# Performance work log

Hardware: AMD Instinct MI355X
Metric: run time of the kernel (lower is better)

The kernel has to match this reference:

```python
import jax, jax.numpy as jnp
import numpy as np

SEQ = 400      # hardcoded per-batch node count in head_splitter
HEADS = 10     # hardcoded num_heads
EPS = 1e-5     # torch LayerNorm default eps


def setup_inputs() -> dict:
    key = jax.random.key(0)
    ks = jax.random.split(key, 6)
    in_dim = out_dim = 640
    N = 25600  # 64 batches * 400 nodes
    x = jax.random.normal(ks[0], (N, in_dim), dtype=jnp.float32)
    # nn.Linear(in, out, bias=False) weights have shape [out, in]; y = x @ W.T
    s = 1.0 / np.sqrt(in_dim)
    Wq = jax.random.uniform(ks[1], (out_dim, in_dim), jnp.float32, -s, s)
    Wk = jax.random.uniform(ks[2], (out_dim, in_dim), jnp.float32, -s, s)
    Wv = jax.random.uniform(ks[3], (out_dim, in_dim), jnp.float32, -s, s)
    gamma = jnp.ones((out_dim,), jnp.float32)
    beta = jnp.zeros((out_dim,), jnp.float32)
    return {"x": x, "Wq": Wq, "Wk": Wk, "Wv": Wv, "gamma": gamma, "beta": beta}


def reference(x, Wq, Wk, Wv, gamma, beta):
    N, D = x.shape
    B = N // SEQ
    dk = D // HEADS
    Q = x @ Wq.T
    K = x @ Wk.T
    V = x @ Wv.T
    # head_splitter: per-batch raw reshape [SEQ, D] -> (HEADS, SEQ, dk), stacked
    # == raw reshape of the full contiguous tensor [N, D] -> (B, HEADS, SEQ, dk)
    Qh = Q.reshape(B, HEADS, SEQ, dk)
    Vh = V.reshape(B, HEADS, SEQ, dk)
    # NOTE: original uses torch.reshape (NOT transpose) to get (B, H, dk, SEQ)
    Kh = K.reshape(B, HEADS, SEQ, dk).reshape(B, HEADS, dk, SEQ)
    scale = 1.0 / jnp.sqrt(jnp.float32(dk))
    scores = jnp.einsum('bhqd,bhdk->bhqk', Qh, Kh) * scale  # [B,H,SEQ,SEQ]
    w = jax.nn.softmax(scores, axis=-1)
    vals = jnp.einsum('bhqk,bhkd->bhqd', w, Vh)  # [B,H,SEQ,dk]
    # raw row-major reshape back to [N, D], as in the original
    y = vals.reshape(N, D) + x
    mu = jnp.mean(y, axis=-1, keepdims=True)
    var = jnp.mean(jnp.square(y - mu), axis=-1, keepdims=True)
    return (y - mu) * jax.lax.rsqrt(var + EPS) * gamma + beta
```

## Files before the change

### kernel.cpp

```cpp
#include <hip/hip_runtime.h>
#include <hip/hip_bf16.h>


typedef unsigned short u16;
typedef short s8v __attribute__((ext_vector_type(8)));
typedef float f4v __attribute__((ext_vector_type(4)));
typedef u16  u4v __attribute__((ext_vector_type(4)));
typedef u16  u8v __attribute__((ext_vector_type(8)));

__device__ __forceinline__ float us2f(u16 u) {
    union { float f; unsigned int i; } v; v.i = ((unsigned int)u) << 16; return v.f;
}
__device__ __forceinline__ u16 f2us(float f) {
    __hip_bfloat16 h = __float2bfloat16(f);
    return *reinterpret_cast<u16*>(&h);
}
__device__ __forceinline__ s8v ld8f(const float* p) {
    const float4 a = ((const float4*)p)[0], b = ((const float4*)p)[1];
    s8v r;
    r[0] = (short)f2us(a.x); r[1] = (short)f2us(a.y);
    r[2] = (short)f2us(a.z); r[3] = (short)f2us(a.w);
    r[4] = (short)f2us(b.x); r[5] = (short)f2us(b.y);
    r[6] = (short)f2us(b.z); r[7] = (short)f2us(b.w);
    return r;
}
__device__ __forceinline__ void gload16(const u16* g, u16* l) {
    u16* gm = const_cast<u16*>(g);
    __builtin_amdgcn_global_load_lds(
        (__attribute__((address_space(1))) unsigned int*)gm,
        (__attribute__((address_space(3))) unsigned int*)l, 16, 0, 0);
}


__global__ __launch_bounds__(256)
void cvt(const float* __restrict__ Wq, const float* __restrict__ Wk,
         const float* __restrict__ Wv, const float* __restrict__ x,
         u16* __restrict__ Wb, u16* __restrict__ xb)
{
    const int g = blockIdx.x * 256 + threadIdx.x;
    if (g < 153600) {
        const float* src = (g < 51200) ? Wq : (g < 102400) ? Wk : Wv;
        const int rem = g % 51200;
        *(s8v*)(Wb + (size_t)g * 8) = ld8f(src + (size_t)rem * 8);
    } else {
        const int gx = g - 153600;
        *(s8v*)(xb + (size_t)gx * 8) = ld8f(x + (size_t)gx * 8);
    }
}

#define QKV_LDS 36864
__global__ __launch_bounds__(256, 4)
void qkv(const u16* __restrict__ xb, const u16* __restrict__ Wb,
         u16* __restrict__ Qb, u16* __restrict__ Kb, u16* __restrict__ Vb)
{
    extern __shared__ u16 qsm[];
    u16* As = qsm;
    u16* Bs = qsm + 8192;
    const int bx = blockIdx.x;
    const int sw = (bx & 7) * 375 + (bx >> 3);
    const int mt = sw / 15, nt = sw % 15;
    const int m0 = mt * 128, n0 = nt * 128;
    const int t = threadIdx.x, lane = t & 63, w = t >> 6;
    const int l15 = lane & 15, quad = lane >> 4;
    const int wr = w >> 1, wc = w & 1;

    f4v acc[4][4];
    #pragma unroll
    for (int a = 0; a < 4; ++a)
        #pragma unroll
        for (int b = 0; b < 4; ++b) acc[a][b] = (f4v){0.f, 0.f, 0.f, 0.f};

    for (int k0 = 0; k0 < 640; k0 += 64) {
        __syncthreads();
        #pragma unroll
        for (int j = 0; j < 4; ++j) {
            const int c  = (w * 4 + j) * 64 + lane;
            const int rg = c >> 3;
            const int sg = (c & 7) ^ (rg & 7);
            gload16(xb + (size_t)(m0 + rg) * 640 + k0 + sg * 8,
                    As + (w * 4 + j) * 512);
            gload16(Wb + (size_t)(n0 + rg) * 640 + k0 + sg * 8,
                    Bs + (w * 4 + j) * 512);
        }
        __syncthreads();

        #pragma unroll
        for (int kk = 0; kk < 2; ++kk) {
            s8v af[4], bf[4];
            #pragma unroll
            for (int mi = 0; mi < 4; ++mi) {
                const int row = wr * 64 + mi * 16 + l15;
                const int s   = kk * 4 + quad;
                af[mi] = *(const s8v*)(As + ((row * 8 + (s ^ (row & 7))) << 3));
            }
            #pragma unroll
            for (int ni = 0; ni < 4; ++ni) {
                const int row = wc * 64 + ni * 16 + l15;
                const int s   = kk * 4 + quad;
                bf[ni] = *(const s8v*)(Bs + ((row * 8 + (s ^ (row & 7))) << 3));
            }
            #pragma unroll
            for (int mi = 0; mi < 4; ++mi)
                #pragma unroll
                for (int ni = 0; ni < 4; ++ni)
                    acc[mi][ni] = __builtin_amdgcn_mfma_f32_16x16x32_bf16(
                        af[mi], bf[ni], acc[mi][ni], 0, 0, 0);
        }
    }

    __syncthreads();
    u16* Cs = qsm;
    #pragma unroll
    for (int mi = 0; mi < 4; ++mi)
        #pragma unroll
        for (int ni = 0; ni < 4; ++ni)
            #pragma unroll
            for (int i = 0; i < 4; ++i) {
                const int row = wr * 64 + mi * 16 + quad * 4 + i;
                const int col = wc * 64 + ni * 16 + l15;
                Cs[row * 144 + col] = f2us(acc[mi][ni][i]);
            }
    __syncthreads();
    const int mat = (n0 >= 1280) ? 2 : (n0 >= 640 ? 1 : 0);
    u16* dst = (mat == 0) ? Qb : (mat == 1 ? Kb : Vb);
    const int lc0 = n0 - mat * 640;
    #pragma unroll
    for (int j2 = 0; j2 < 8; ++j2) {
        const int cl  = t + 256 * j2;
        const int row = cl >> 4, cg = cl & 15;
        const s8v v = *(const s8v*)(Cs + row * 144 + cg * 8);
        *(s8v*)(dst + (size_t)(m0 + row) * 640 + lc0 + cg * 8) = v;
    }
}

__global__ __launch_bounds__(256)
void kvt(const u16* __restrict__ Kb, const u16* __restrict__ Vb,
         u16* __restrict__ Ktg, u16* __restrict__ Vtg)
{
    extern __shared__ u16 sm[];
    const int bh = blockIdx.x, t = threadIdx.x;
    {
        const u16* src = Kb + (size_t)bh * 25600;
        for (int c = t; c < 3200; c += 256) {
            const int d = c / 50, k8 = (c % 50) * 8;
            *(s8v*)(sm + ((d * 512 + k8) ^ (((d >> 3) & 7) << 3))) =
                *(const s8v*)(src + (size_t)c * 8);
        }
        __syncthreads();
        u16* o = Ktg + (size_t)bh * 25600;
        for (int c = t; c < 3200; c += 256) {
            const int key = c >> 3, d0 = (c & 7) * 8;
            u8v v;
            #pragma unroll
            for (int j = 0; j < 8; ++j) {
                const int d = d0 + j;
                v[j] = sm[(d * 512 + key) ^ (((d >> 3) & 7) << 3)];
            }
            *(u8v*)(o + key * 64 + d0) = v;
        }
    }
    __syncthreads();
    {
        const u16* src = Vb + (size_t)bh * 25600;
        for (int c = t; c < 3200; c += 256) {
            const int key = c >> 3, d0 = (c & 7) * 8;
            *(s8v*)(sm + ((key * 64 + d0) ^ (((key >> 3) & 7) << 3))) =
                *(const s8v*)(src + (size_t)c * 8);
        }
        __syncthreads();
        u16* o = Vtg + (size_t)bh * 26624;
        for (int c = t; c < 3584; c += 256) {
            const int d = ((c >> 3) & 7) + (((c >> 6) & 7) << 3);
            const int s = (c & 7) + ((c >> 9) << 3);
            if (s >= 52) continue;
            const int key0 = s * 8;
            u8v v;
            #pragma unroll
            for (int j = 0; j < 8; ++j) {
                const int key = key0 + j;
                v[j] = (key < 400)
                     ? sm[(key * 64 + d) ^ (((key >> 3) & 7) << 3)] : (u16)0;
            }
            *(u8v*)(o + d * 416 + key0) = v;
        }
    }
}

#define ATTN_LDS 44320
__global__ __launch_bounds__(512, 6)
void attn(const u16* __restrict__ Qb, const u16* __restrict__ Ktg,
          const u16* __restrict__ Vtg, const float* __restrict__ x,
          const float* __restrict__ gamma, const float* __restrict__ beta,
          float* __restrict__ out)
{
    extern __shared__ char smem[];
    u16*   Pb  = (u16*)smem;
    float* Vl  = (float*)(smem + 33920);
    float* rs_ = (float*)(smem + 44160);

    const int bx = blockIdx.x;
    const int sw = (bx & 7) * 800 + (bx >> 3);
    const int bh = sw / 10, qc = sw % 10;
    const int t = threadIdx.x, lane = t & 63, w = t >> 6;
    const int l15 = lane & 15, quad = lane >> 4;
    const size_t kbase = (size_t)bh * 25600;
    const size_t vbase = (size_t)bh * 26624;
    const size_t qoff0 = kbase + (size_t)qc * 2560;
    const int M0[3] = {0, 16, 24};

    s8v qf[3][2];
    #pragma unroll
    for (int mt = 0; mt < 3; ++mt)
        #pragma unroll
        for (int kq = 0; kq < 2; ++kq)
            qf[mt][kq] = *(const s8v*)(Qb + qoff0
                         + (size_t)(M0[mt] + l15) * 64 + kq * 32 + quad * 8);

    int nts[4]; int nn = 0;
    for (int nt = w; nt < 25; nt += 8) nts[nn++] = nt;
    s8v k0c, k1c;
    {
        const u16* kp = Ktg + kbase + (size_t)(nts[0] * 16 + l15) * 64 + quad * 8;
        k0c = *(const s8v*)(kp); k1c = *(const s8v*)(kp + 32);
    }
    #pragma unroll
    for (int j = 0; j < 4; ++j) {
        if (j >= nn) break;
        s8v k0n = k0c, k1n = k1c;
        if (j + 1 < nn) {
            const u16* kp = Ktg + kbase
                          + (size_t)(nts[j + 1] * 16 + l15) * 64 + quad * 8;
            k0n = *(const s8v*)(kp); k1n = *(const s8v*)(kp + 32);
        }
        const int nt = nts[j];
        #pragma unroll
        for (int mt = 0; mt < 3; ++mt) {
            f4v acc = (f4v){0.f, 0.f, 0.f, 0.f};
            acc = __builtin_amdgcn_mfma_f32_16x16x32_bf16(k0c, qf[mt][0], acc, 0, 0, 0);
            acc = __builtin_amdgcn_mfma_f32_16x16x32_bf16(k1c, qf[mt][1], acc, 0, 0, 0);
            u4v pv;
            #pragma unroll
            for (int i = 0; i < 4; ++i)
                pv[i] = f2us(__expf(acc[i] * 0.125f));
            *(u4v*)(Pb + (M0[mt] + l15) * 424 + nt * 16 + quad * 4) = pv;
        }
        k0c = k0n; k1c = k1n;
    }
    __syncthreads();

    for (int q = w; q < 40; q += 8) {
        const int c0 = lane * 8;
        float s = 0.f;
        if (c0 < 400) {
            const s8v pvv = *(const s8v*)(Pb + q * 424 + c0);
            #pragma unroll
            for (int j = 0; j < 8; ++j) s += us2f((u16)pvv[j]);
        } else if (c0 < 424) {
            *(u8v*)(Pb + q * 424 + c0) = (u8v){0,0,0,0,0,0,0,0};
        }
        #pragma unroll
        for (int off = 32; off; off >>= 1) s += __shfl_xor(s, off);
        if (lane == 0) rs_[q] = 1.0f / s;
    }
    __syncthreads();

    {
        const int ntv = w & 3;
        const int mA  = w >> 2;
        const bool two = (mA == 0);
        f4v acc0 = (f4v){0.f, 0.f, 0.f, 0.f};
        f4v acc1 = (f4v){0.f, 0.f, 0.f, 0.f};
        const u16* vp  = Vtg + vbase + (size_t)(ntv * 16 + l15) * 416 + quad * 8;
        const u16* pa  = Pb + (M0[mA] + l15) * 424 + quad * 8;
        const u16* pa2 = Pb + (24 + l15) * 424 + quad * 8;
        s8v bc  = *(const s8v*)(vp);
        s8v p0c = *(const s8v*)(pa);
        s8v p2c = two ? *(const s8v*)(pa2) : p0c;
        #pragma unroll
        for (int k0 = 0; k0 < 416; k0 += 32) {
            s8v bn = bc, p0n = p0c, p2n = p2c;
            if (k0 + 32 < 416) {
                bn  = *(const s8v*)(vp + k0 + 32);
                p0n = *(const s8v*)(pa + k0 + 32);
                if (two) p2n = *(const s8v*)(pa2 + k0 + 32);
            }
            acc0 = __builtin_amdgcn_mfma_f32_16x16x32_bf16(p0c, bc, acc0, 0, 0, 0);
            if (two)
                acc1 = __builtin_amdgcn_mfma_f32_16x16x32_bf16(p2c, bc, acc1, 0, 0, 0);
            bc = bn; p0c = p0n; p2c = p2n;
        }
        #pragma unroll
        for (int i = 0; i < 4; ++i) {
            Vl[(M0[mA] + quad * 4 + i) * 64 + ntv * 16 + l15] = acc0[i];
            if (two) Vl[(24 + quad * 4 + i) * 64 + ntv * 16 + l15] = acc1[i];
        }
    }
    __syncthreads();

    if (w < 4) {
        const size_t grow = ((size_t)bh * 40 + qc * 4 + w) * 640;
        float xv[10], vl[10], rr[10], gv[10], bv[10];
        #pragma unroll
        for (int ci = 0; ci < 10; ++ci) {
            const int col = lane + 64 * ci;
            xv[ci] = x[grow + col];
            gv[ci] = gamma[col];
            bv[ci] = beta[col];
            vl[ci] = Vl[w * 640 + col];
            rr[ci] = rs_[w * 10 + ci];
        }
        float y[10], s = 0.f, ss = 0.f;
        #pragma unroll
        for (int ci = 0; ci < 10; ++ci) {
            const float v = vl[ci] * rr[ci] + xv[ci];
            y[ci] = v; s += v; ss += v * v;
        }
        #pragma unroll
        for (int off = 32; off; off >>= 1) {
            s += __shfl_xor(s, off); ss += __shfl_xor(ss, off);
        }
        const float mu = s * (1.f / 640.f);
        float var = ss * (1.f / 640.f) - mu * mu;
        var = fmaxf(var, 0.f);
        const float rstd = rsqrtf(var + 1e-5f);
        #pragma unroll
        for (int ci = 0; ci < 10; ++ci) {
            const int col = lane + 64 * ci;
            out[grow + col] = (y[ci] - mu) * rstd * gv[ci] + bv[ci];
        }
    }
}

#define LDS_BYTES 163712

template<int MODE>
__global__ __launch_bounds__(1024, 4)
void mha(const float* __restrict__ x,
         const float* __restrict__ Wq, const float* __restrict__ Wk,
         const float* __restrict__ Wv,
         const float* __restrict__ gamma, const float* __restrict__ beta,
         float* __restrict__ out,
         const u16* __restrict__ Wb, u16* __restrict__ Qb)
{
    extern __shared__ char smem[];
    u16*   Kt  = (u16*)(smem);
    u16*   Vt  = (u16*)(smem + 57600);
    u16*   Xs  = (u16*)(smem + 111872);
    u16*   Pb  = (u16*)(smem + 111872);
    float* Vl  = (float*)(smem + 145792);
    float* rs_ = (float*)(smem + 156032);

    const int    bh   = blockIdx.x;
    const size_t base = (size_t)bh * 25600;
    const int    t    = threadIdx.x;
    const int    lane = t & 63;
    const int    w    = t >> 6;
    const int    l15  = lane & 15;
    const int    quad = lane >> 4;

    for (int i = t; i < 6400; i += 1024) {
        const int row = i / 160, col = (i % 160) * 4;
        const float4 v = *(const float4*)(x + base + row * 640 + col);
        *(u4v*)(Xs + row * 648 + col) =
            (u4v){f2us(v.x), f2us(v.y), f2us(v.z), f2us(v.w)};
    }
    for (int i = t; i < 64 * 24; i += 1024)
        Vt[(i / 24) * 424 + 400 + (i % 24)] = 0;
    __syncthreads();

    {
        const int M0a[3] = {0, 16, 24};
        int nts[3], nnt = 0;
        for (int nt = w; nt < 40; nt += 16) nts[nnt++] = nt;

        for (int zi = 0; zi < 3; ++zi) {
            const float* Wsrc = (zi == 0) ? Wq : (zi == 1) ? Wk : Wv;
            f4v acc[3][3];
            #pragma unroll
            for (int a = 0; a < 3; ++a)
                #pragma unroll
                for (int b = 0; b < 3; ++b) acc[a][b] = (f4v){0.f,0.f,0.f,0.f};

            for (int k0 = 0; k0 < 640; k0 += 32) {
                s8v afr[3];
                #pragma unroll
                for (int mt = 0; mt < 3; ++mt)
                    afr[mt] = *(const s8v*)(Xs + (M0a[mt] + l15) * 648 + k0 + quad * 8);
                #pragma unroll
                for (int nk = 0; nk < 3; ++nk) {
                    if (nk >= nnt) break;
                    const int nt = nts[nk];
                    s8v bfr;
                    if (MODE == 0)
                        bfr = *(const s8v*)(Wb + (size_t)zi * 409600
                                            + (nt * 16 + l15) * 640 + k0 + quad * 8);
                    else
                        bfr = ld8f(Wsrc + (size_t)(nt * 16 + l15) * 640 + k0 + quad * 8);
                    #pragma unroll
                    for (int mt = 0; mt < 3; ++mt)
                        acc[nk][mt] = __builtin_amdgcn_mfma_f32_16x16x32_bf16(
                            afr[mt], bfr, acc[nk][mt], 0, 0, 0);
                }
            }
            #pragma unroll
            for (int nk = 0; nk < 3; ++nk) {
                if (nk >= nnt) break;
                #pragma unroll
                for (int mt = 0; mt < 3; ++mt)
                    #pragma unroll
                    for (int i = 0; i < 4; ++i) {
                        const int r  = M0a[mt] + quad * 4 + i;
                        const int oc = nts[nk] * 16 + l15;
                        const int f  = r * 640 + oc;
                        const float v = acc[nk][mt][i];
                        if (zi == 0) {
                            if (MODE == 0) Qb[base + f] = f2us(v);
                            else           out[base + f] = v;
                        } else if (zi == 1) {
                            const int d = f / 400, key = f - d * 400;
                            Kt[key * 72 + d] = f2us(v);
                        } else {
                            Vt[(f & 63) * 424 + (f >> 6)] = f2us(v);
                        }
                    }
            }
        }
    }
    __syncthreads();

    const int M0b[3] = {0, 16, 24};
    for (int qc = 0; qc < 10; ++qc) {
        for (int nt = w; nt < 25; nt += 16) {
            s8v bfr[2];
            #pragma unroll
            for (int kq = 0; kq < 2; ++kq)
                bfr[kq] = *(const s8v*)(Kt + (nt * 16 + l15) * 72 + kq * 32 + quad * 8);
            #pragma unroll
            for (int mt = 0; mt < 3; ++mt) {
                f4v acc = (f4v){0.f, 0.f, 0.f, 0.f};
                #pragma unroll
                for (int kq = 0; kq < 2; ++kq) {
                    const size_t qoff = base + (size_t)qc * 2560
                                      + (M0b[mt] + l15) * 64 + kq * 32 + quad * 8;
                    s8v a = (MODE == 0) ? *(const s8v*)(Qb + qoff) : ld8f(out + qoff);
                    acc = __builtin_amdgcn_mfma_f32_16x16x32_bf16(a, bfr[kq], acc, 0, 0, 0);
                }
                #pragma unroll
                for (int i = 0; i < 4; ++i)
                    Pb[(M0b[mt] + quad * 4 + i) * 424 + nt * 16 + l15] =
                        f2us(acc[i] * 0.125f);
            }
        }
        __syncthreads();

        for (int q = w; q < 40; q += 16) {
            float sv[7], m = -1e30f;
            #pragma unroll
            for (int ii = 0; ii < 7; ++ii) {
                const int c = lane + ii * 64;
                sv[ii] = (c < 400) ? us2f(Pb[q * 424 + c]) : -1e30f;
                m = fmaxf(m, sv[ii]);
            }
            #pragma unroll
            for (int off = 32; off; off >>= 1) m = fmaxf(m, __shfl_xor(m, off));
            float s = 0.f;
            #pragma unroll
            for (int ii = 0; ii < 7; ++ii) {
                const int c = lane + ii * 64;
                const float e = (c < 400) ? __expf(sv[ii] - m) : 0.f;
                s += e;
                if (c < 424) Pb[q * 424 + c] = f2us(e);
            }
            #pragma unroll
            for (int off = 32; off; off >>= 1) s += __shfl_xor(s, off);
            if (lane == 0) rs_[q] = s;
        }
        __syncthreads();

        if (w < 12) {
            const int mt = w >> 2, nt = w & 3;
            f4v acc = (f4v){0.f, 0.f, 0.f, 0.f};
            for (int k0 = 0; k0 < 416; k0 += 32) {
                s8v a = *(const s8v*)(Pb + (M0b[mt] + l15) * 424 + k0 + quad * 8);
                s8v b = *(const s8v*)(Vt + (nt * 16 + l15) * 424 + k0 + quad * 8);
                acc = __builtin_amdgcn_mfma_f32_16x16x32_bf16(a, b, acc, 0, 0, 0);
            }
            #pragma unroll
            for (int i = 0; i < 4; ++i)
                Vl[(M0b[mt] + quad * 4 + i) * 64 + nt * 16 + l15] = acc[i];
        }
        __syncthreads();

        if (w < 4) {
            const int    r    = qc * 4 + w;
            const size_t grow = base + (size_t)r * 640;
            float y[10], s = 0.f, ss = 0.f;
            #pragma unroll
            for (int ci = 0; ci < 10; ++ci) {
                const int col = lane + 64 * ci;
                const float v = Vl[w * 640 + col] / rs_[w * 10 + ci] + x[grow + col];
                y[ci] = v; s += v; ss += v * v;
            }
            #pragma unroll
            for (int off = 32; off; off >>= 1) {
                s += __shfl_xor(s, off); ss += __shfl_xor(ss, off);
            }
            const float mu = s * (1.f / 640.f);
            float var = ss * (1.f / 640.f) - mu * mu;
            var = fmaxf(var, 0.f);
            const float rstd = rsqrtf(var + 1e-5f);
            #pragma unroll
            for (int ci = 0; ci < 10; ++ci) {
                const int col = lane + 64 * ci;
                out[grow + col] = (y[ci] - mu) * rstd * gamma[col] + beta[col];
            }
        }
    }
}

__global__ __launch_bounds__(256)
void wconv(const float* __restrict__ Wq, const float* __restrict__ Wk,
           const float* __restrict__ Wv, u16* __restrict__ Wb)
{
    const int g = blockIdx.x * 256 + threadIdx.x;
    const float* src = (g < 51200) ? Wq : (g < 102400) ? Wk : Wv;
    const int rem = g % 51200;
    *(s8v*)(Wb + (size_t)g * 8) = ld8f(src + (size_t)rem * 8);
}

extern "C" void kernel_launch(void* const* d_in, const int* in_sizes, int n_in,
                              void* d_out, int out_size, void* d_ws, size_t ws_size,
                              hipStream_t stream)
{
    const float* x     = (const float*)d_in[0];
    const float* Wq    = (const float*)d_in[1];
    const float* Wk    = (const float*)d_in[2];
    const float* Wv    = (const float*)d_in[3];
    const float* gamma = (const float*)d_in[4];
    const float* beta  = (const float*)d_in[5];
    float* out = (float*)d_out;
    (void)in_sizes; (void)n_in; (void)out_size;

    hipFuncSetAttribute(reinterpret_cast<const void*>(&qkv),
                        hipFuncAttributeMaxDynamicSharedMemorySize, QKV_LDS);
    hipFuncSetAttribute(reinterpret_cast<const void*>(&kvt),
                        hipFuncAttributeMaxDynamicSharedMemorySize, 65536);
    hipFuncSetAttribute(reinterpret_cast<const void*>(&attn),
                        hipFuncAttributeMaxDynamicSharedMemorySize, ATTN_LDS);
    hipFuncSetAttribute(reinterpret_cast<const void*>(&mha<0>),
                        hipFuncAttributeMaxDynamicSharedMemorySize, LDS_BYTES);
    hipFuncSetAttribute(reinterpret_cast<const void*>(&mha<1>),
                        hipFuncAttributeMaxDynamicSharedMemorySize, LDS_BYTES);

    const size_t NEED_NEW = 200376320ull;

    if (ws_size >= NEED_NEW) {
        u16* Wb  = (u16*)d_ws;
        u16* xb  = Wb  + 1228800;
        u16* Qb  = xb  + 16384000;
        u16* Kb  = Qb  + 16384000;
        u16* Vb  = Kb  + 16384000;
        u16* Ktg = Vb  + 16384000;
        u16* Vtg = Ktg + 16384000;
        cvt <<<8600, 256, 0, stream>>>(Wq, Wk, Wv, x, Wb, xb);
        qkv <<<3000, 256, QKV_LDS, stream>>>(xb, Wb, Qb, Kb, Vb);
        kvt <<<640,  256, 65536, stream>>>(Kb, Vb, Ktg, Vtg);
        attn<<<6400, 512, ATTN_LDS, stream>>>(Qb, Ktg, Vtg, x, gamma, beta, out);
    } else if (ws_size >= (size_t)(2457600 + 32768000)) {
        u16* Wb = (u16*)d_ws;
        u16* Qb = Wb + 1228800;
        wconv<<<600, 256, 0, stream>>>(Wq, Wk, Wv, Wb);
        mha<0><<<640, 1024, LDS_BYTES, stream>>>(x, Wq, Wk, Wv, gamma, beta, out, Wb, Qb);
    } else {
        mha<1><<<640, 1024, LDS_BYTES, stream>>>(x, Wq, Wk, Wv, gamma, beta, out,
                                                 (const u16*)d_ws, (u16*)d_ws);
    }
}
```

Baseline: 349.6 us.

## Fuse softmax row sums into exp pass, split kvt, prefetch residual rows

The transpose kernel now launches twice as many blocks, one block per head doing either the K or the V transpose, so the two halves run in parallel. In the attention kernel, softmax denominators are accumulated in registers during the exp pass and combined with shuffles and LDS atomics. This removes the separate pass that re-read the P tile to sum rows. Residual x rows are loaded at kernel start to hide their latency, and normalization moves to the upper four waves. The row sums use fp32 exponentials instead of the rounded bf16 values, which slightly changes numerics, and x registers stay live across the whole kernel, which may raise register pressure.

```diff
diff --git a/kernel.cpp b/kernel.cpp
--- a/kernel.cpp
+++ b/kernel.cpp
@@ -138,8 +138,8 @@
          u16* __restrict__ Ktg, u16* __restrict__ Vtg)
 {
     extern __shared__ u16 sm[];
-    const int bh = blockIdx.x, t = threadIdx.x;
-    {
+    const int bh = blockIdx.x >> 1, t = threadIdx.x;
+    if ((blockIdx.x & 1) == 0) {
         const u16* src = Kb + (size_t)bh * 25600;
         for (int c = t; c < 3200; c += 256) {
             const int d = c / 50, k8 = (c % 50) * 8;
@@ -158,9 +158,7 @@
             }
             *(u8v*)(o + key * 64 + d0) = v;
         }
-    }
-    __syncthreads();
-    {
+    } else {
         const u16* src = Vb + (size_t)bh * 25600;
         for (int c = t; c < 3200; c += 256) {
             const int key = c >> 3, d0 = (c & 7) * 8;
@@ -208,6 +206,17 @@
     const size_t qoff0 = kbase + (size_t)qc * 2560;
     const int M0[3] = {0, 16, 24};
 
+    const int    xr    = w & 3;
+    const size_t growp = ((size_t)bh * 40 + qc * 4 + xr) * 640;
+    float xv[10];
+    #pragma unroll
+    for (int ci = 0; ci < 10; ++ci) xv[ci] = x[growp + lane + 64 * ci];
+
+    if (t < 40) rs_[t] = 0.f;
+    for (int i = t; i < 960; i += 512)
+        Pb[(i / 24) * 424 + 400 + (i % 24)] = 0;
+    __syncthreads();
+
     s8v qf[3][2];
     #pragma unroll
     for (int mt = 0; mt < 3; ++mt)
@@ -223,6 +232,7 @@
         const u16* kp = Ktg + kbase + (size_t)(nts[0] * 16 + l15) * 64 + quad * 8;
         k0c = *(const s8v*)(kp); k1c = *(const s8v*)(kp + 32);
     }
+    float ps[3] = {0.f, 0.f, 0.f};
     #pragma unroll
     for (int j = 0; j < 4; ++j) {
         if (j >= nn) break;
@@ -240,27 +250,24 @@
             acc = __builtin_amdgcn_mfma_f32_16x16x32_bf16(k1c, qf[mt][1], acc, 0, 0, 0);
             u4v pv;
             #pragma unroll
-            for (int i = 0; i < 4; ++i)
-                pv[i] = f2us(__expf(acc[i] * 0.125f));
+            for (int i = 0; i < 4; ++i) {
+                const float e = __expf(acc[i] * 0.125f);
+                pv[i] = f2us(e);
+                ps[mt] += e;
+            }
             *(u4v*)(Pb + (M0[mt] + l15) * 424 + nt * 16 + quad * 4) = pv;
         }
         k0c = k0n; k1c = k1n;
     }
-    __syncthreads();
-
-    for (int q = w; q < 40; q += 8) {
-        const int c0 = lane * 8;
-        float s = 0.f;
-        if (c0 < 400) {
-            const s8v pvv = *(const s8v*)(Pb + q * 424 + c0);
-            #pragma unroll
-            for (int j = 0; j < 8; ++j) s += us2f((u16)pvv[j]);
-        } else if (c0 < 424) {
-            *(u8v*)(Pb + q * 424 + c0) = (u8v){0,0,0,0,0,0,0,0};
-        }
-        #pragma unroll
-        for (int off = 32; off; off >>= 1) s += __shfl_xor(s, off);
-        if (lane == 0) rs_[q] = 1.0f / s;
+    #pragma unroll
+    for (int mt = 0; mt < 3; ++mt) {
+        ps[mt] += __shfl_xor(ps[mt], 16);
+        ps[mt] += __shfl_xor(ps[mt], 32);
+    }
+    if (quad == 0) {
+        atomicAdd(&rs_[l15],      ps[0]);
+        atomicAdd(&rs_[16 + l15], ps[1]);
+        if (l15 >= 8) atomicAdd(&rs_[24 + l15], ps[2]);
     }
     __syncthreads();
 
@@ -297,22 +304,22 @@
     }
     __syncthreads();
 
-    if (w < 4) {
-        const size_t grow = ((size_t)bh * 40 + qc * 4 + w) * 640;
-        float xv[10], vl[10], rr[10], gv[10], bv[10];
+    if (w >= 4) {
+        const int r = w - 4;
+        const size_t grow = growp;
+        float vl[10], rr[10], gv[10], bv[10];
         #pragma unroll
         for (int ci = 0; ci < 10; ++ci) {
             const int col = lane + 64 * ci;
-            xv[ci] = x[grow + col];
             gv[ci] = gamma[col];
             bv[ci] = beta[col];
-            vl[ci] = Vl[w * 640 + col];
-            rr[ci] = rs_[w * 10 + ci];
+            vl[ci] = Vl[r * 640 + col];
+            rr[ci] = rs_[r * 10 + ci];
         }
         float y[10], s = 0.f, ss = 0.f;
         #pragma unroll
         for (int ci = 0; ci < 10; ++ci) {
-            const float v = vl[ci] * rr[ci] + xv[ci];
+            const float v = vl[ci] / rr[ci] + xv[ci];
             y[ci] = v; s += v; ss += v * v;
         }
         #pragma unroll
@@ -564,7 +571,7 @@
         u16* Vtg = Ktg + 16384000;
         cvt <<<8600, 256, 0, stream>>>(Wq, Wk, Wv, x, Wb, xb);
         qkv <<<3000, 256, QKV_LDS, stream>>>(xb, Wb, Qb, Kb, Vb);
-        kvt <<<640,  256, 65536, stream>>>(Kb, Vb, Ktg, Vtg);
+        kvt <<<1280, 256, 65536, stream>>>(Kb, Vb, Ktg, Vtg);
         attn<<<6400, 512, ATTN_LDS, stream>>>(Qb, Ktg, Vtg, x, gamma, beta, out);
     } else if (ws_size >= (size_t)(2457600 + 32768000)) {
         u16* Wb = (u16*)d_ws;
```

Measured after the change: 371.5 us. 1.06x slower.
